# Optimization experiments

Measured on AMD Instinct MI355X. Metric: run time of the kernel, lower is better.

Reference implementation:

```python
import jax, jax.numpy as jnp
import numpy as np

B, LS, LL = 1024, 128, 2048
E, VOCAB = 16, 160000
NH, KD = 8, 6
LSH_DIM, TOPK = 16, 48
D_ITEM = 3 * E  # 48
EPS = 1e-3  # keras LayerNormalization default epsilon


def setup_inputs() -> dict:
    key = jax.random.key(0)
    ks = iter(jax.random.split(key, 64))
    def nk():
        return next(ks)
    def ids(shape):
        return jax.random.randint(nk(), shape, 0, VOCAB, dtype=jnp.int32)
    inp = {}
    for n in ['uid', 'utag1', 'utag2', 'utag3', 'utag4',
              'label_goods_ids', 'label_shop_ids', 'label_cate_ids']:
        inp[n] = ids((B,))
    for n in ['shortterm_goods_ids', 'shortterm_shop_ids', 'shortterm_cate_ids']:
        inp[n] = ids((B, LS))
    for n in ['longterm_goods_ids', 'longterm_shop_ids', 'longterm_cate_ids']:
        inp[n] = ids((B, LL))
    def rn(shape, s=0.05):
        return (jax.random.normal(nk(), shape) * s).astype(jnp.float32)
    inp['emb_table'] = rn((VOCAB, E))
    inp['H'] = rn((D_ITEM, LSH_DIM), 1.0)  # non-trainable random projection
    for p in ('s', 'l'):
        inp[p + 'Wq'] = rn((D_ITEM, NH, KD)); inp[p + 'bq'] = jnp.zeros((NH, KD), jnp.float32)
        inp[p + 'Wk'] = rn((D_ITEM, NH, KD)); inp[p + 'bk'] = jnp.zeros((NH, KD), jnp.float32)
        inp[p + 'Wv'] = rn((D_ITEM, NH, KD)); inp[p + 'bv'] = jnp.zeros((NH, KD), jnp.float32)
        inp[p + 'Wo'] = rn((NH, KD, D_ITEM)); inp[p + 'bo'] = jnp.zeros((D_ITEM,), jnp.float32)
    Din = D_ITEM + 5 * E + D_ITEM + D_ITEM  # 224
    inp['W1'] = rn((Din, 200)); inp['b1'] = jnp.zeros((200,), jnp.float32)
    inp['g1'] = jnp.ones((200,), jnp.float32); inp['be1'] = jnp.zeros((200,), jnp.float32)
    inp['W2'] = rn((200, 80)); inp['b2'] = jnp.zeros((80,), jnp.float32)
    inp['g2'] = jnp.ones((80,), jnp.float32); inp['be2'] = jnp.zeros((80,), jnp.float32)
    inp['W3'] = rn((80, 1)); inp['b3'] = jnp.zeros((1,), jnp.float32)
    return inp


def _ln(x, g, b):
    m = jnp.mean(x, axis=-1, keepdims=True)
    v = jnp.mean((x - m) ** 2, axis=-1, keepdims=True)
    return (x - m) * jax.lax.rsqrt(v + EPS) * g + b


def _mha(q, kv, mask3, Wq, bq, Wk, bk, Wv, bv, Wo, bo):
    # q: [B,1,D], kv: [B,K,D], mask3: [B,1,K] float (1=keep)
    qh = jnp.einsum('bqe,ehd->bqhd', q, Wq) + bq
    kh = jnp.einsum('bke,ehd->bkhd', kv, Wk) + bk
    vh = jnp.einsum('bke,ehd->bkhd', kv, Wv) + bv
    sc = jnp.einsum('bqhd,bkhd->bhqk', qh, kh) / jnp.sqrt(jnp.float32(KD))
    sc = sc + (1.0 - mask3[:, None, :, :]) * jnp.float32(-1e9)
    a = jax.nn.softmax(sc, axis=-1)
    o = jnp.einsum('bhqk,bkhd->bqhd', a, vh)
    return jnp.einsum('bqhd,hde->bqe', o, Wo) + bo


def reference(uid, utag1, utag2, utag3, utag4,
              label_goods_ids, label_shop_ids, label_cate_ids,
              shortterm_goods_ids, shortterm_shop_ids, shortterm_cate_ids,
              longterm_goods_ids, longterm_shop_ids, longterm_cate_ids,
              emb_table, H,
              sWq, sbq, sWk, sbk, sWv, sbv, sWo, sbo,
              lWq, lbq, lWk, lbk, lWv, lbv, lWo, lbo,
              W1, b1, g1, be1, W2, b2, g2, be2, W3, b3):
    short_mask = shortterm_goods_ids == 0  # padding_index == 0
    long_mask = longterm_goods_ids == 0

    def stack_embed(lst):
        X = jnp.stack([t if t.ndim == 2 else t[:, None] for t in lst], axis=2)  # [B,L,F]
        Xe = emb_table[X]  # [B,L,F,E]
        return Xe.reshape(Xe.shape[0], Xe.shape[1], -1)

    X_item = stack_embed([label_goods_ids, label_shop_ids, label_cate_ids])  # [B,1,48]
    X_user = stack_embed([uid, utag1, utag2, utag3, utag4])                  # [B,1,80]
    X_short = stack_embed([shortterm_goods_ids, shortterm_shop_ids, shortterm_cate_ids])  # [B,LS,48]
    X_long = stack_embed([longterm_goods_ids, longterm_shop_ids, longterm_cate_ids])      # [B,LL,48]

    # short-term interest
    slen = jnp.sum((~short_mask).astype(jnp.int32), axis=1)
    smask = (jnp.arange(LS)[None, :] < slen[:, None]).astype(jnp.float32)[:, None, :]
    short_int = _mha(X_item, X_short, smask, sWq, sbq, sWk, sbk, sWv, sbv, sWo, sbo)[:, 0]

    # long-term interest: LSH sign-hash hamming top-k retrieval
    series_codes = jnp.sign(jnp.einsum('ble,em->blm', X_long, H))  # [B,LL,16]
    item_codes = jnp.sign(jnp.einsum('ble,em->blm', X_item, H))    # [B,1,16]
    scores = jnp.sum((series_codes == item_codes).astype(jnp.float32), axis=-1)  # [B,LL]
    scores = jnp.where(long_mask, -jnp.inf, scores)
    _, idx = jax.lax.top_k(scores, TOPK)  # descending, padded entries last
    top_emb = jnp.take_along_axis(X_long, idx[:, :, None], axis=1)  # [B,TOPK,48]
    top_mask = jnp.take_along_axis(long_mask, idx, axis=1)
    llen = jnp.sum((~top_mask).astype(jnp.int32), axis=1)
    lmask = (jnp.arange(TOPK)[None, :] < llen[:, None]).astype(jnp.float32)[:, None, :]
    long_int = _mha(X_item, top_emb, lmask, lWq, lbq, lWk, lbk, lWv, lbv, lWo, lbo)[:, 0]

    x = jnp.concatenate([X_item[:, 0], X_user[:, 0], short_int, long_int], axis=1)  # [B,224]
    h1 = jax.nn.relu(_ln(x @ W1 + b1, g1, be1))
    h2 = jax.nn.relu(_ln(h1 @ W2 + b2, g2, be2))
    out = jax.nn.sigmoid(h2 @ W3 + b3)  # [B,1]
    return out
```

## Files before the change

### kernel.cpp

```cpp
#include <hip/hip_runtime.h>
#include <math.h>

#define BB 1024
#define LSx 128
#define LLx 2048
#define TOPKx 48

__global__ __launch_bounds__(256, 8) void k_score(
    const int* __restrict__ lg, const int* __restrict__ lsh, const int* __restrict__ lc,
    const int* __restrict__ ig, const int* __restrict__ ish, const int* __restrict__ ici,
    const float* __restrict__ emb, const float* __restrict__ Hm,
    signed char* __restrict__ gsc)
{
  __shared__ float Xitem[48];
  __shared__ int icode[16];
  __shared__ float4 xsh[256][4];
  const int b = blockIdx.y, tid = threadIdx.x;

  const int l = blockIdx.x * 256 + tid;
  const size_t off = (size_t)b * LLx + l;
  const int gid = lg[off];

  if (tid < 48) {
    const int seg = tid >> 4, e = tid & 15;
    const int id = (seg == 0) ? ig[b] : (seg == 1) ? ish[b] : ici[b];
    Xitem[tid] = emb[(size_t)id * 16 + e];
  }
  __syncthreads();
  if (tid < 16) {
    float dd = 0.f;
    for (int e = 0; e < 48; ++e) dd += Xitem[e] * Hm[e * 16 + tid];
    icode[tid] = (dd > 0.f) ? 1 : (dd < 0.f ? -1 : 0);
  }

  float d[16];
  #pragma unroll
  for (int m = 0; m < 16; ++m) d[m] = 0.f;

  const int srow = tid >> 2;
  const int q = tid & 3;
  const size_t bbase = (size_t)b * LLx + (size_t)blockIdx.x * 256;

  #pragma unroll
  for (int seg = 0; seg < 3; ++seg) {
    const int* idarr = (seg == 0) ? lg : (seg == 1) ? lsh : lc;
    #pragma unroll
    for (int jj = 0; jj < 4; ++jj) {
      const int pos = jj * 64 + srow;
      const int id = idarr[bbase + pos];
      const float4 v = *(const float4*)(emb + (size_t)id * 16 + q * 4);
      xsh[pos][q ^ ((pos >> 1) & 3)] = v;
    }
    __syncthreads();
    if (gid != 0) {
      float x[16];
      #pragma unroll
      for (int qq = 0; qq < 4; ++qq) {
        const float4 r = xsh[tid][qq ^ ((tid >> 1) & 3)];
        x[qq * 4 + 0] = r.x; x[qq * 4 + 1] = r.y;
        x[qq * 4 + 2] = r.z; x[qq * 4 + 3] = r.w;
      }
      const float* hb = Hm + seg * 256;
      #pragma unroll
      for (int i = 0; i < 16; ++i) {
        const float xi = x[i];
        #pragma unroll
        for (int mc = 0; mc < 4; ++mc) {
          const float4 h4 = *(const float4*)(hb + i * 16 + mc * 4);
          d[mc * 4 + 0] += xi * h4.x;
          d[mc * 4 + 1] += xi * h4.y;
          d[mc * 4 + 2] += xi * h4.z;
          d[mc * 4 + 3] += xi * h4.w;
        }
      }
    }
    if (seg < 2) __syncthreads();
  }

  int sc = -1;
  if (gid != 0) {
    sc = 0;
    #pragma unroll
    for (int m = 0; m < 16; ++m) {
      const int cs = (d[m] > 0.f) ? 1 : (d[m] < 0.f ? -1 : 0);
      sc += (cs == icode[m]) ? 1 : 0;
    }
  }
  gsc[off] = (signed char)sc;
}

template<int K, int STRIDE, bool IS_LONG>
__global__ __launch_bounds__(128) void k_mha(
    const int* __restrict__ kg, const int* __restrict__ ks, const int* __restrict__ kc,
    const int* __restrict__ ig, const int* __restrict__ ish, const int* __restrict__ ici,
    const float* __restrict__ emb,
    const float* __restrict__ Wq, const float* __restrict__ bq,
    const float* __restrict__ Wk, const float* __restrict__ bk,
    const float* __restrict__ Wv, const float* __restrict__ bv,
    const float* __restrict__ Wo, const float* __restrict__ bo,
    const int* __restrict__ sel,
    float* __restrict__ outv)
{
  __shared__ float Xitem[48];
  __shared__ float qh[48];
  __shared__ __align__(16) float vhs[K][48];
  __shared__ float scs[8][K + 4];
  __shared__ float osm[48];
  __shared__ unsigned char validf[K];
  const int b = blockIdx.x, tid = threadIdx.x;

  if (tid < 48) {
    const int seg = tid >> 4, e = tid & 15;
    const int id = (seg == 0) ? ig[b] : (seg == 1) ? ish[b] : ici[b];
    Xitem[tid] = emb[(size_t)id * 16 + e];
  }
  __syncthreads();
  if (tid < 48) {
    float a = bq[tid];
    for (int e = 0; e < 48; ++e) a += Xitem[e] * Wq[e * 48 + tid];
    qh[tid] = a;
  }

  int gid = 0, sid = 0, cid = 0;
  if (tid < K) {
    const int pos = IS_LONG ? sel[b * TOPKx + tid] : tid;
    const size_t off = (size_t)b * STRIDE + pos;
    gid = kg[off]; sid = ks[off]; cid = kc[off];
  }
  const int nval = __syncthreads_count((tid < K) && (gid != 0));

  if (tid < K) {
    validf[tid] = IS_LONG ? (unsigned char)(gid != 0) : (unsigned char)(tid < nval);
    float kh[48], vh[48];
    #pragma unroll
    for (int j = 0; j < 48; ++j) { kh[j] = bk[j]; vh[j] = bv[j]; }
    const int ids3[3] = {gid, sid, cid};
    #pragma unroll
    for (int seg = 0; seg < 3; ++seg) {
      const float* row = emb + (size_t)ids3[seg] * 16;
      #pragma unroll
      for (int i4 = 0; i4 < 4; ++i4) {
        const float4 xv = ((const float4*)row)[i4];
        const float xs[4] = {xv.x, xv.y, xv.z, xv.w};
        #pragma unroll
        for (int c = 0; c < 4; ++c) {
          const int e = seg * 16 + i4 * 4 + c;
          const float* wkr = Wk + e * 48;
          const float* wvr = Wv + e * 48;
          const float xe = xs[c];
          #pragma unroll
          for (int j = 0; j < 48; ++j) {
            kh[j] += xe * wkr[j];
            vh[j] += xe * wvr[j];
          }
        }
      }
    }
    #pragma unroll
    for (int h = 0; h < 8; ++h) {
      float s = 0.f;
      #pragma unroll
      for (int d = 0; d < 6; ++d) s += qh[h * 6 + d] * kh[h * 6 + d];
      scs[h][tid] = s * 0.40824829046386301637f;
    }
    #pragma unroll
    for (int j = 0; j < 48; ++j) vhs[tid][j] = vh[j];
  }
  __syncthreads();

  {
    const int h = tid >> 4, l16 = tid & 15;
    float amax = -INFINITY;
    for (int k = l16; k < K; k += 16) if (validf[k]) amax = fmaxf(amax, scs[h][k]);
    #pragma unroll
    for (int m = 1; m < 16; m <<= 1) amax = fmaxf(amax, __shfl_xor(amax, m, 16));
    if (nval == 0) {
      for (int k = l16; k < K; k += 16) scs[h][k] = 1.0f / (float)K;
    } else {
      float ssum = 0.f;
      for (int k = l16; k < K; k += 16) {
        const float ev = validf[k] ? expf(scs[h][k] - amax) : 0.f;
        scs[h][k] = ev;
        ssum += ev;
      }
      #pragma unroll
      for (int m = 1; m < 16; m <<= 1) ssum += __shfl_xor(ssum, m, 16);
      const float inv = 1.0f / ssum;
      for (int k = l16; k < K; k += 16) scs[h][k] *= inv;
    }
  }
  __syncthreads();

  if (tid < 48) {
    const int h = tid / 6;
    float a = 0.f;
    for (int k = 0; k < K; ++k) a += scs[h][k] * vhs[k][tid];
    osm[tid] = a;
  }
  __syncthreads();
  if (tid < 48) {
    float r = bo[tid];
    for (int j = 0; j < 48; ++j) r += osm[j] * Wo[j * 48 + tid];
    outv[b * 48 + tid] = r;
  }
}

__global__ __launch_bounds__(256) void k_mha_long(
    const int* __restrict__ kg, const int* __restrict__ ks, const int* __restrict__ kc,
    const int* __restrict__ ig, const int* __restrict__ ish, const int* __restrict__ ici,
    const float* __restrict__ emb,
    const float* __restrict__ Wq, const float* __restrict__ bq,
    const float* __restrict__ Wk, const float* __restrict__ bk,
    const float* __restrict__ Wv, const float* __restrict__ bv,
    const float* __restrict__ Wo, const float* __restrict__ bo,
    const signed char* __restrict__ gsc,
    float* __restrict__ outv)
{
  __shared__ int hist[18];
  __shared__ int cnt_above;
  __shared__ int wsum[4];
  __shared__ int selsh[TOPKx];
  __shared__ float Xitem[48];
  __shared__ float qh[48];
  __shared__ __align__(16) float vhs[TOPKx][48];
  __shared__ float scs[8][TOPKx + 4];
  __shared__ float osm[48];
  __shared__ unsigned char validf[TOPKx];
  const int b = blockIdx.x, tid = threadIdx.x;

  const int2 myv = ((const int2*)(gsc + (size_t)b * LLx))[tid];
  signed char loc[8];
  *(int2*)loc = myv;

  if (tid < 18) hist[tid] = 0;
  if (tid == 0) cnt_above = 0;
  if (tid < 48) {
    const int seg = tid >> 4, e = tid & 15;
    const int id = (seg == 0) ? ig[b] : (seg == 1) ? ish[b] : ici[b];
    Xitem[tid] = emb[(size_t)id * 16 + e];
  }
  __syncthreads();

  #pragma unroll
  for (int j = 0; j < 8; ++j) atomicAdd(&hist[(int)loc[j] + 1], 1);
  if (tid < 48) {
    float a = bq[tid];
    for (int e = 0; e < 48; ++e) a += Xitem[e] * Wq[e * 48 + tid];
    qh[tid] = a;
  }
  __syncthreads();

  int above = 0, tval = -1, need = 0;
  for (int s = 16; s >= -1; --s) {
    const int c = hist[s + 1];
    if (above + c >= TOPKx) { tval = s; need = TOPKx - above; break; }
    above += c;
  }

  const int base_l = tid * (LLx / 256);
  int cnt = 0;
  #pragma unroll
  for (int j = 0; j < 8; ++j) cnt += ((int)loc[j] == tval) ? 1 : 0;
  int v = cnt;
  const int lane = tid & 63, wave = tid >> 6;
  #pragma unroll
  for (int o = 1; o < 64; o <<= 1) {
    const int u = __shfl_up(v, o, 64);
    if (lane >= o) v += u;
  }
  if (lane == 63) wsum[wave] = v;
  __syncthreads();
  int rank = v - cnt;
  for (int w = 0; w < wave; ++w) rank += wsum[w];

  #pragma unroll
  for (int j = 0; j < 8; ++j) {
    const int l = base_l + j;
    const int s = (int)loc[j];
    if (s > tval) {
      const int slot = atomicAdd(&cnt_above, 1);
      selsh[slot] = l;
    } else if (s == tval) {
      if (rank < need) selsh[above + rank] = l;
      ++rank;
    }
  }
  __syncthreads();

  int gid = 0, sid = 0, cid = 0;
  if (tid < TOPKx) {
    const int pos = selsh[tid];
    const size_t off = (size_t)b * LLx + pos;
    gid = kg[off]; sid = ks[off]; cid = kc[off];
  }
  const int nval = __syncthreads_count((tid < TOPKx) && (gid != 0));

  if (tid < TOPKx) {
    validf[tid] = (unsigned char)(gid != 0);
    float kh[48], vh[48];
    #pragma unroll
    for (int j = 0; j < 48; ++j) { kh[j] = bk[j]; vh[j] = bv[j]; }
    const int ids3[3] = {gid, sid, cid};
    #pragma unroll
    for (int seg = 0; seg < 3; ++seg) {
      const float* row = emb + (size_t)ids3[seg] * 16;
      #pragma unroll
      for (int i4 = 0; i4 < 4; ++i4) {
        const float4 xv = ((const float4*)row)[i4];
        const float xs[4] = {xv.x, xv.y, xv.z, xv.w};
        #pragma unroll
        for (int c = 0; c < 4; ++c) {
          const int e = seg * 16 + i4 * 4 + c;
          const float* wkr = Wk + e * 48;
          const float* wvr = Wv + e * 48;
          const float xe = xs[c];
          #pragma unroll
          for (int j = 0; j < 48; ++j) {
            kh[j] += xe * wkr[j];
            vh[j] += xe * wvr[j];
          }
        }
      }
    }
    #pragma unroll
    for (int h = 0; h < 8; ++h) {
      float s = 0.f;
      #pragma unroll
      for (int d = 0; d < 6; ++d) s += qh[h * 6 + d] * kh[h * 6 + d];
      scs[h][tid] = s * 0.40824829046386301637f;
    }
    #pragma unroll
    for (int j = 0; j < 48; ++j) vhs[tid][j] = vh[j];
  }
  __syncthreads();

  if (tid < 128) {
    const int h = tid >> 4, l16 = tid & 15;
    float amax = -INFINITY;
    for (int k = l16; k < TOPKx; k += 16) if (validf[k]) amax = fmaxf(amax, scs[h][k]);
    #pragma unroll
    for (int m = 1; m < 16; m <<= 1) amax = fmaxf(amax, __shfl_xor(amax, m, 16));
    if (nval == 0) {
      for (int k = l16; k < TOPKx; k += 16) scs[h][k] = 1.0f / (float)TOPKx;
    } else {
      float ssum = 0.f;
      for (int k = l16; k < TOPKx; k += 16) {
        const float ev = validf[k] ? expf(scs[h][k] - amax) : 0.f;
        scs[h][k] = ev;
        ssum += ev;
      }
      #pragma unroll
      for (int m = 1; m < 16; m <<= 1) ssum += __shfl_xor(ssum, m, 16);
      const float inv = 1.0f / ssum;
      for (int k = l16; k < TOPKx; k += 16) scs[h][k] *= inv;
    }
  }
  __syncthreads();

  if (tid < 48) {
    const int h = tid / 6;
    float a = 0.f;
    for (int k = 0; k < TOPKx; ++k) a += scs[h][k] * vhs[k][tid];
    osm[tid] = a;
  }
  __syncthreads();
  if (tid < 48) {
    float r = bo[tid];
    for (int j = 0; j < 48; ++j) r += osm[j] * Wo[j * 48 + tid];
    outv[b * 48 + tid] = r;
  }
}

__device__ __forceinline__ float block_sum256(float v, float* red) {
  #pragma unroll
  for (int m = 32; m >= 1; m >>= 1) v += __shfl_xor(v, m, 64);
  const int lane = threadIdx.x & 63, wave = threadIdx.x >> 6;
  if (lane == 0) red[wave] = v;
  __syncthreads();
  const float t = red[0] + red[1] + red[2] + red[3];
  __syncthreads();
  return t;
}

__global__ __launch_bounds__(256) void k_mlp(
    const int* __restrict__ uid, const int* __restrict__ u1, const int* __restrict__ u2,
    const int* __restrict__ u3, const int* __restrict__ u4,
    const int* __restrict__ ig, const int* __restrict__ ish, const int* __restrict__ ici,
    const float* __restrict__ emb,
    const float* __restrict__ sint, const float* __restrict__ lint,
    const float* __restrict__ W1, const float* __restrict__ b1,
    const float* __restrict__ g1, const float* __restrict__ be1,
    const float* __restrict__ W2, const float* __restrict__ b2,
    const float* __restrict__ g2, const float* __restrict__ be2,
    const float* __restrict__ W3, const float* __restrict__ b3,
    float* __restrict__ out)
{
  __shared__ __align__(16) float x[224];
  __shared__ __align__(16) float h1[200];
  __shared__ float h2[80];
  __shared__ float red[4];
  const int b = blockIdx.x, tid = threadIdx.x;

  if (tid < 128) {
    const int e = tid & 15;
    int id;
    if (tid < 48) {
      const int seg = tid >> 4;
      id = (seg == 0) ? ig[b] : (seg == 1) ? ish[b] : ici[b];
    } else {
      const int f = (tid - 48) >> 4;
      id = (f == 0) ? uid[b] : (f == 1) ? u1[b] : (f == 2) ? u2[b] : (f == 3) ? u3[b] : u4[b];
    }
    x[tid] = emb[(size_t)id * 16 + e];
  } else if (tid < 176) {
    x[tid] = sint[b * 48 + (tid - 128)];
  } else if (tid < 224) {
    x[tid] = lint[b * 48 + (tid - 176)];
  }
  __syncthreads();

  float v = 0.f;
  if (tid < 200) {
    v = b1[tid];
    for (int i4 = 0; i4 < 56; ++i4) {
      const float4 xv = *(const float4*)(x + i4 * 4);
      const float* w = W1 + i4 * 4 * 200 + tid;
      v += xv.x * w[0];
      v += xv.y * w[200];
      v += xv.z * w[400];
      v += xv.w * w[600];
    }
  }
  const float mean1 = block_sum256((tid < 200) ? v : 0.f, red) * (1.0f / 200.0f);
  const float dv = (tid < 200) ? (v - mean1) : 0.f;
  const float var1 = block_sum256(dv * dv, red) * (1.0f / 200.0f);
  if (tid < 200) {
    const float y = (v - mean1) * rsqrtf(var1 + 1e-3f) * g1[tid] + be1[tid];
    h1[tid] = fmaxf(y, 0.f);
  }
  __syncthreads();

  float v2 = 0.f;
  if (tid < 80) {
    v2 = b2[tid];
    for (int i4 = 0; i4 < 50; ++i4) {
      const float4 xv = *(const float4*)(h1 + i4 * 4);
      const float* w = W2 + i4 * 4 * 80 + tid;
      v2 += xv.x * w[0];
      v2 += xv.y * w[80];
      v2 += xv.z * w[160];
      v2 += xv.w * w[240];
    }
  }
  const float mean2 = block_sum256((tid < 80) ? v2 : 0.f, red) * (1.0f / 80.0f);
  const float dv2 = (tid < 80) ? (v2 - mean2) : 0.f;
  const float var2 = block_sum256(dv2 * dv2, red) * (1.0f / 80.0f);
  if (tid < 80) {
    const float y = (v2 - mean2) * rsqrtf(var2 + 1e-3f) * g2[tid] + be2[tid];
    h2[tid] = fmaxf(y, 0.f);
  }
  __syncthreads();

  const float p = (tid < 80) ? h2[tid] * W3[tid] : 0.f;
  const float z = block_sum256(p, red);
  if (tid == 0) {
    out[b] = 1.0f / (1.0f + expf(-(z + b3[0])));
  }
}

extern "C" void kernel_launch(void* const* d_in, const int* in_sizes, int n_in,
                              void* d_out, int out_size, void* d_ws, size_t ws_size,
                              hipStream_t stream) {
  (void)in_sizes; (void)n_in; (void)out_size; (void)ws_size;
  const int* uid = (const int*)d_in[0];
  const int* u1  = (const int*)d_in[1];
  const int* u2  = (const int*)d_in[2];
  const int* u3  = (const int*)d_in[3];
  const int* u4  = (const int*)d_in[4];
  const int* ig  = (const int*)d_in[5];
  const int* ish = (const int*)d_in[6];
  const int* ici = (const int*)d_in[7];
  const int* sg  = (const int*)d_in[8];
  const int* ss  = (const int*)d_in[9];
  const int* scd = (const int*)d_in[10];
  const int* lg  = (const int*)d_in[11];
  const int* ls  = (const int*)d_in[12];
  const int* lcd = (const int*)d_in[13];
  const float* emb = (const float*)d_in[14];
  const float* Hm  = (const float*)d_in[15];
  const float* sWq = (const float*)d_in[16];
  const float* sbq = (const float*)d_in[17];
  const float* sWk = (const float*)d_in[18];
  const float* sbk = (const float*)d_in[19];
  const float* sWv = (const float*)d_in[20];
  const float* sbv = (const float*)d_in[21];
  const float* sWo = (const float*)d_in[22];
  const float* sbo = (const float*)d_in[23];
  const float* lWq = (const float*)d_in[24];
  const float* lbq = (const float*)d_in[25];
  const float* lWk = (const float*)d_in[26];
  const float* lbk = (const float*)d_in[27];
  const float* lWv = (const float*)d_in[28];
  const float* lbv = (const float*)d_in[29];
  const float* lWo = (const float*)d_in[30];
  const float* lbo = (const float*)d_in[31];
  const float* W1 = (const float*)d_in[32];
  const float* b1 = (const float*)d_in[33];
  const float* g1 = (const float*)d_in[34];
  const float* be1 = (const float*)d_in[35];
  const float* W2 = (const float*)d_in[36];
  const float* b2 = (const float*)d_in[37];
  const float* g2 = (const float*)d_in[38];
  const float* be2 = (const float*)d_in[39];
  const float* W3 = (const float*)d_in[40];
  const float* b3 = (const float*)d_in[41];
  float* out = (float*)d_out;

  signed char* gsc = (signed char*)d_ws;
  float* sint = (float*)((char*)d_ws + (size_t)BB * LLx);
  float* lint = sint + BB * 48;

  k_score<<<dim3(LLx / 256, BB), dim3(256), 0, stream>>>(
      lg, ls, lcd, ig, ish, ici, emb, Hm, gsc);
  k_mha<128, 128, false><<<dim3(BB), dim3(128), 0, stream>>>(
      sg, ss, scd, ig, ish, ici, emb,
      sWq, sbq, sWk, sbk, sWv, sbv, sWo, sbo, (const int*)nullptr, sint);
  k_mha_long<<<dim3(BB), dim3(256), 0, stream>>>(
      lg, ls, lcd, ig, ish, ici, emb,
      lWq, lbq, lWk, lbk, lWv, lbv, lWo, lbo, gsc, lint);
  k_mlp<<<dim3(BB), dim3(256), 0, stream>>>(
      uid, u1, u2, u3, u4, ig, ish, ici, emb,
      sint, lint, W1, b1, g1, be1, W2, b2, g2, be2, W3, b3, out);
}
```

Measured before the change: 354.2 us.

## Prefetch next segment gathers in scoring and split K/V projection across more threads

In the LSH scoring kernel, the embedding gathers for the next segment are now issued into registers before the current segment's projection is computed. This overlaps gather latency with the matmul, and the occupancy hint in the launch bounds is dropped to make room for the extra registers. The short-term MHA kernel goes from 128 to 256 threads, with each half computing 24 of the 48 K/V columns. The long-term MHA kernel uses all 4 wave-groups of 64 threads to compute 12 columns each instead of letting only 48 threads work. This cuts per-thread serial work and register pressure, at the cost of redundant embedding-row loads across thread groups.

```diff
diff --git a/kernel.cpp b/kernel.cpp
--- a/kernel.cpp
+++ b/kernel.cpp
@@ -6,7 +6,7 @@
 #define LLx 2048
 #define TOPKx 48
 
-__global__ __launch_bounds__(256, 8) void k_score(
+__global__ __launch_bounds__(256) void k_score(
     const int* __restrict__ lg, const int* __restrict__ lsh, const int* __restrict__ lc,
     const int* __restrict__ ig, const int* __restrict__ ish, const int* __restrict__ ici,
     const float* __restrict__ emb, const float* __restrict__ Hm,
@@ -33,25 +33,39 @@
     icode[tid] = (dd > 0.f) ? 1 : (dd < 0.f ? -1 : 0);
   }
 
-  float d[16];
-  #pragma unroll
-  for (int m = 0; m < 16; ++m) d[m] = 0.f;
-
   const int srow = tid >> 2;
   const int q = tid & 3;
   const size_t bbase = (size_t)b * LLx + (size_t)blockIdx.x * 256;
 
+  float4 stage[4];
+  #pragma unroll
+  for (int jj = 0; jj < 4; ++jj) {
+    const int pos = jj * 64 + srow;
+    const int id = lg[bbase + pos];
+    stage[jj] = *(const float4*)(emb + (size_t)id * 16 + q * 4);
+  }
+
+  float d[16];
+  #pragma unroll
+  for (int m = 0; m < 16; ++m) d[m] = 0.f;
+
   #pragma unroll
   for (int seg = 0; seg < 3; ++seg) {
-    const int* idarr = (seg == 0) ? lg : (seg == 1) ? lsh : lc;
     #pragma unroll
     for (int jj = 0; jj < 4; ++jj) {
       const int pos = jj * 64 + srow;
-      const int id = idarr[bbase + pos];
-      const float4 v = *(const float4*)(emb + (size_t)id * 16 + q * 4);
-      xsh[pos][q ^ ((pos >> 1) & 3)] = v;
+      xsh[pos][q ^ ((pos >> 1) & 3)] = stage[jj];
     }
     __syncthreads();
+    if (seg < 2) {
+      const int* idn = (seg == 0) ? lsh : lc;
+      #pragma unroll
+      for (int jj = 0; jj < 4; ++jj) {
+        const int pos = jj * 64 + srow;
+        const int id = idn[bbase + pos];
+        stage[jj] = *(const float4*)(emb + (size_t)id * 16 + q * 4);
+      }
+    }
     if (gid != 0) {
       float x[16];
       #pragma unroll
@@ -89,8 +103,7 @@
   gsc[off] = (signed char)sc;
 }
 
-template<int K, int STRIDE, bool IS_LONG>
-__global__ __launch_bounds__(128) void k_mha(
+__global__ __launch_bounds__(256) void k_mha_short(
     const int* __restrict__ kg, const int* __restrict__ ks, const int* __restrict__ kc,
     const int* __restrict__ ig, const int* __restrict__ ish, const int* __restrict__ ici,
     const float* __restrict__ emb,
@@ -98,16 +111,17 @@
     const float* __restrict__ Wk, const float* __restrict__ bk,
     const float* __restrict__ Wv, const float* __restrict__ bv,
     const float* __restrict__ Wo, const float* __restrict__ bo,
-    const int* __restrict__ sel,
     float* __restrict__ outv)
 {
   __shared__ float Xitem[48];
   __shared__ float qh[48];
-  __shared__ __align__(16) float vhs[K][48];
-  __shared__ float scs[8][K + 4];
+  __shared__ __align__(16) float vhs[LSx][48];
+  __shared__ float scs[8][LSx + 4];
   __shared__ float osm[48];
-  __shared__ unsigned char validf[K];
+  __shared__ unsigned char validf[LSx];
   const int b = blockIdx.x, tid = threadIdx.x;
+  const int w = tid >> 7;
+  const int k = tid & 127;
 
   if (tid < 48) {
     const int seg = tid >> 4, e = tid & 15;
@@ -121,19 +135,19 @@
     qh[tid] = a;
   }
 
-  int gid = 0, sid = 0, cid = 0;
-  if (tid < K) {
-    const int pos = IS_LONG ? sel[b * TOPKx + tid] : tid;
-    const size_t off = (size_t)b * STRIDE + pos;
+  int gid, sid, cid;
+  {
+    const size_t off = (size_t)b * LSx + k;
     gid = kg[off]; sid = ks[off]; cid = kc[off];
   }
-  const int nval = __syncthreads_count((tid < K) && (gid != 0));
-
-  if (tid < K) {
-    validf[tid] = IS_LONG ? (unsigned char)(gid != 0) : (unsigned char)(tid < nval);
-    float kh[48], vh[48];
-    #pragma unroll
-    for (int j = 0; j < 48; ++j) { kh[j] = bk[j]; vh[j] = bv[j]; }
+  const int nval = __syncthreads_count((w == 0) && (gid != 0));
+  if (w == 0) validf[k] = (unsigned char)(k < nval);
+
+  {
+    const int cb = w * 24;
+    float kh[24], vh[24];
+    #pragma unroll
+    for (int j = 0; j < 24; ++j) { kh[j] = bk[cb + j]; vh[j] = bv[cb + j]; }
     const int ids3[3] = {gid, sid, cid};
     #pragma unroll
     for (int seg = 0; seg < 3; ++seg) {
@@ -145,11 +159,11 @@
         #pragma unroll
         for (int c = 0; c < 4; ++c) {
           const int e = seg * 16 + i4 * 4 + c;
-          const float* wkr = Wk + e * 48;
-          const float* wvr = Wv + e * 48;
+          const float* wkr = Wk + e * 48 + cb;
+          const float* wvr = Wv + e * 48 + cb;
           const float xe = xs[c];
           #pragma unroll
-          for (int j = 0; j < 48; ++j) {
+          for (int j = 0; j < 24; ++j) {
             kh[j] += xe * wkr[j];
             vh[j] += xe * wvr[j];
           }
@@ -157,36 +171,37 @@
       }
     }
     #pragma unroll
-    for (int h = 0; h < 8; ++h) {
+    for (int hh = 0; hh < 4; ++hh) {
+      const int h = w * 4 + hh;
       float s = 0.f;
       #pragma unroll
-      for (int d = 0; d < 6; ++d) s += qh[h * 6 + d] * kh[h * 6 + d];
-      scs[h][tid] = s * 0.40824829046386301637f;
-    }
-    #pragma unroll
-    for (int j = 0; j < 48; ++j) vhs[tid][j] = vh[j];
-  }
-  __syncthreads();
-
-  {
+      for (int d = 0; d < 6; ++d) s += qh[h * 6 + d] * kh[hh * 6 + d];
+      scs[h][k] = s * 0.40824829046386301637f;
+    }
+    #pragma unroll
+    for (int j = 0; j < 24; ++j) vhs[k][cb + j] = vh[j];
+  }
+  __syncthreads();
+
+  if (tid < 128) {
     const int h = tid >> 4, l16 = tid & 15;
     float amax = -INFINITY;
-    for (int k = l16; k < K; k += 16) if (validf[k]) amax = fmaxf(amax, scs[h][k]);
+    for (int kk = l16; kk < LSx; kk += 16) if (validf[kk]) amax = fmaxf(amax, scs[h][kk]);
     #pragma unroll
     for (int m = 1; m < 16; m <<= 1) amax = fmaxf(amax, __shfl_xor(amax, m, 16));
     if (nval == 0) {
-      for (int k = l16; k < K; k += 16) scs[h][k] = 1.0f / (float)K;
+      for (int kk = l16; kk < LSx; kk += 16) scs[h][kk] = 1.0f / (float)LSx;
     } else {
       float ssum = 0.f;
-      for (int k = l16; k < K; k += 16) {
-        const float ev = validf[k] ? expf(scs[h][k] - amax) : 0.f;
-        scs[h][k] = ev;
+      for (int kk = l16; kk < LSx; kk += 16) {
+        const float ev = validf[kk] ? expf(scs[h][kk] - amax) : 0.f;
+        scs[h][kk] = ev;
         ssum += ev;
       }
       #pragma unroll
       for (int m = 1; m < 16; m <<= 1) ssum += __shfl_xor(ssum, m, 16);
       const float inv = 1.0f / ssum;
-      for (int k = l16; k < K; k += 16) scs[h][k] *= inv;
+      for (int kk = l16; kk < LSx; kk += 16) scs[h][kk] *= inv;
     }
   }
   __syncthreads();
@@ -194,7 +209,7 @@
   if (tid < 48) {
     const int h = tid / 6;
     float a = 0.f;
-    for (int k = 0; k < K; ++k) a += scs[h][k] * vhs[k][tid];
+    for (int k2 = 0; k2 < LSx; ++k2) a += scs[h][k2] * vhs[k2][tid];
     osm[tid] = a;
   }
   __syncthreads();
@@ -287,19 +302,22 @@
   }
   __syncthreads();
 
+  const int g = tid >> 6;
+  const int kk = tid & 63;
   int gid = 0, sid = 0, cid = 0;
-  if (tid < TOPKx) {
-    const int pos = selsh[tid];
+  if (kk < TOPKx) {
+    const int pos = selsh[kk];
     const size_t off = (size_t)b * LLx + pos;
     gid = kg[off]; sid = ks[off]; cid = kc[off];
   }
-  const int nval = __syncthreads_count((tid < TOPKx) && (gid != 0));
-
-  if (tid < TOPKx) {
-    validf[tid] = (unsigned char)(gid != 0);
-    float kh[48], vh[48];
-    #pragma unroll
-    for (int j = 0; j < 48; ++j) { kh[j] = bk[j]; vh[j] = bv[j]; }
+  const int nval = __syncthreads_count((g == 0) && (kk < TOPKx) && (gid != 0));
+
+  if (kk < TOPKx) {
+    if (g == 0) validf[kk] = (unsigned char)(gid != 0);
+    const int cb = g * 12;
+    float kh[12], vh[12];
+    #pragma unroll
+    for (int j = 0; j < 12; ++j) { kh[j] = bk[cb + j]; vh[j] = bv[cb + j]; }
     const int ids3[3] = {gid, sid, cid};
     #pragma unroll
     for (int seg = 0; seg < 3; ++seg) {
@@ -311,11 +329,11 @@
         #pragma unroll
         for (int c = 0; c < 4; ++c) {
           const int e = seg * 16 + i4 * 4 + c;
-          const float* wkr = Wk + e * 48;
-          const float* wvr = Wv + e * 48;
+          const float* wkr = Wk + e * 48 + cb;
+          const float* wvr = Wv + e * 48 + cb;
           const float xe = xs[c];
           #pragma unroll
-          for (int j = 0; j < 48; ++j) {
+          for (int j = 0; j < 12; ++j) {
             kh[j] += xe * wkr[j];
             vh[j] += xe * wvr[j];
           }
@@ -323,14 +341,15 @@
       }
     }
     #pragma unroll
-    for (int h = 0; h < 8; ++h) {
+    for (int hh = 0; hh < 2; ++hh) {
+      const int h = g * 2 + hh;
       float s = 0.f;
       #pragma unroll
-      for (int d = 0; d < 6; ++d) s += qh[h * 6 + d] * kh[h * 6 + d];
-      scs[h][tid] = s * 0.40824829046386301637f;
-    }
-    #pragma unroll
-    for (int j = 0; j < 48; ++j) vhs[tid][j] = vh[j];
+      for (int d = 0; d < 6; ++d) s += qh[h * 6 + d] * kh[hh * 6 + d];
+      scs[h][kk] = s * 0.40824829046386301637f;
+    }
+    #pragma unroll
+    for (int j = 0; j < 12; ++j) vhs[kk][cb + j] = vh[j];
   }
   __syncthreads();
 
@@ -522,9 +541,9 @@
 
   k_score<<<dim3(LLx / 256, BB), dim3(256), 0, stream>>>(
       lg, ls, lcd, ig, ish, ici, emb, Hm, gsc);
-  k_mha<128, 128, false><<<dim3(BB), dim3(128), 0, stream>>>(
+  k_mha_short<<<dim3(BB), dim3(256), 0, stream>>>(
       sg, ss, scd, ig, ish, ici, emb,
-      sWq, sbq, sWk, sbk, sWv, sbv, sWo, sbo, (const int*)nullptr, sint);
+      sWq, sbq, sWk, sbk, sWv, sbv, sWo, sbo, sint);
   k_mha_long<<<dim3(BB), dim3(256), 0, stream>>>(
       lg, ls, lcd, ig, ish, ici, emb,
       lWq, lbq, lWk, lbk, lWv, lbv, lWo, lbo, gsc, lint);
```

Result: slower. 482.9 us (+36.3%).

## Split MHA kernels per head, separate top-k kernel, fold output projection into MLP

Applied to the files above, without the earlier changes.

The attention kernels are re-gridded to one block per (batch, head), so each thread keeps only 6 key/value accumulators instead of 48. This cuts register pressure and raises parallelism. Top-k selection moves into its own kernel that writes indices to global memory, and the Wo output projection moves into the MLP kernel. k_score drops the XOR swizzle in favour of a padded shared array and relaxes its launch bounds occupancy hint. The trade-off is one extra launch, recomputing the per-head query in every block, and extra global traffic for the selection indices.

```diff
diff --git a/kernel.cpp b/kernel.cpp
--- a/kernel.cpp
+++ b/kernel.cpp
@@ -6,7 +6,7 @@
 #define LLx 2048
 #define TOPKx 48
 
-__global__ __launch_bounds__(256, 8) void k_score(
+__global__ __launch_bounds__(256, 2) void k_score(
     const int* __restrict__ lg, const int* __restrict__ lsh, const int* __restrict__ lc,
     const int* __restrict__ ig, const int* __restrict__ ish, const int* __restrict__ ici,
     const float* __restrict__ emb, const float* __restrict__ Hm,
@@ -14,7 +14,7 @@
 {
   __shared__ float Xitem[48];
   __shared__ int icode[16];
-  __shared__ float4 xsh[256][4];
+  __shared__ __align__(16) float4 xsh[256][5];
   const int b = blockIdx.y, tid = threadIdx.x;
 
   const int l = blockIdx.x * 256 + tid;
@@ -33,14 +33,14 @@
     icode[tid] = (dd > 0.f) ? 1 : (dd < 0.f ? -1 : 0);
   }
 
-  float d[16];
-  #pragma unroll
-  for (int m = 0; m < 16; ++m) d[m] = 0.f;
-
   const int srow = tid >> 2;
   const int q = tid & 3;
   const size_t bbase = (size_t)b * LLx + (size_t)blockIdx.x * 256;
 
+  float d[16];
+  #pragma unroll
+  for (int m = 0; m < 16; ++m) d[m] = 0.f;
+
   #pragma unroll
   for (int seg = 0; seg < 3; ++seg) {
     const int* idarr = (seg == 0) ? lg : (seg == 1) ? lsh : lc;
@@ -48,15 +48,14 @@
     for (int jj = 0; jj < 4; ++jj) {
       const int pos = jj * 64 + srow;
       const int id = idarr[bbase + pos];
-      const float4 v = *(const float4*)(emb + (size_t)id * 16 + q * 4);
-      xsh[pos][q ^ ((pos >> 1) & 3)] = v;
+      xsh[pos][q] = *(const float4*)(emb + (size_t)id * 16 + q * 4);
     }
     __syncthreads();
     if (gid != 0) {
       float x[16];
       #pragma unroll
       for (int qq = 0; qq < 4; ++qq) {
-        const float4 r = xsh[tid][qq ^ ((tid >> 1) & 3)];
+        const float4 r = xsh[tid][qq];
         x[qq * 4 + 0] = r.x; x[qq * 4 + 1] = r.y;
         x[qq * 4 + 2] = r.z; x[qq * 4 + 3] = r.w;
       }
@@ -89,25 +88,78 @@
   gsc[off] = (signed char)sc;
 }
 
-template<int K, int STRIDE, bool IS_LONG>
-__global__ __launch_bounds__(128) void k_mha(
+__global__ __launch_bounds__(256) void k_topk(
+    const signed char* __restrict__ gsc, int* __restrict__ sel)
+{
+  __shared__ int hist[18];
+  __shared__ int cnt_above;
+  __shared__ int wsum[4];
+  const int b = blockIdx.x, tid = threadIdx.x;
+
+  const int2 myv = ((const int2*)(gsc + (size_t)b * LLx))[tid];
+  signed char loc[8];
+  *(int2*)loc = myv;
+
+  if (tid < 18) hist[tid] = 0;
+  if (tid == 0) cnt_above = 0;
+  __syncthreads();
+
+  #pragma unroll
+  for (int j = 0; j < 8; ++j) atomicAdd(&hist[(int)loc[j] + 1], 1);
+  __syncthreads();
+
+  int above = 0, tval = -1, need = 0;
+  for (int s = 16; s >= -1; --s) {
+    const int c = hist[s + 1];
+    if (above + c >= TOPKx) { tval = s; need = TOPKx - above; break; }
+    above += c;
+  }
+
+  const int base_l = tid * (LLx / 256);
+  int cnt = 0;
+  #pragma unroll
+  for (int j = 0; j < 8; ++j) cnt += ((int)loc[j] == tval) ? 1 : 0;
+  int v = cnt;
+  const int lane = tid & 63, wave = tid >> 6;
+  #pragma unroll
+  for (int o = 1; o < 64; o <<= 1) {
+    const int u = __shfl_up(v, o, 64);
+    if (lane >= o) v += u;
+  }
+  if (lane == 63) wsum[wave] = v;
+  __syncthreads();
+  int rank = v - cnt;
+  for (int w = 0; w < wave; ++w) rank += wsum[w];
+
+  #pragma unroll
+  for (int j = 0; j < 8; ++j) {
+    const int l = base_l + j;
+    const int s = (int)loc[j];
+    if (s > tval) {
+      const int slot = atomicAdd(&cnt_above, 1);
+      sel[b * TOPKx + slot] = l;
+    } else if (s == tval) {
+      if (rank < need) sel[b * TOPKx + above + rank] = l;
+      ++rank;
+    }
+  }
+}
+
+__global__ __launch_bounds__(128) void k_mha_short_h(
     const int* __restrict__ kg, const int* __restrict__ ks, const int* __restrict__ kc,
     const int* __restrict__ ig, const int* __restrict__ ish, const int* __restrict__ ici,
     const float* __restrict__ emb,
     const float* __restrict__ Wq, const float* __restrict__ bq,
     const float* __restrict__ Wk, const float* __restrict__ bk,
     const float* __restrict__ Wv, const float* __restrict__ bv,
-    const float* __restrict__ Wo, const float* __restrict__ bo,
-    const int* __restrict__ sel,
-    float* __restrict__ outv)
+    float* __restrict__ osm_g)
 {
   __shared__ float Xitem[48];
-  __shared__ float qh[48];
-  __shared__ __align__(16) float vhs[K][48];
-  __shared__ float scs[8][K + 4];
-  __shared__ float osm[48];
-  __shared__ unsigned char validf[K];
-  const int b = blockIdx.x, tid = threadIdx.x;
+  __shared__ float qh[6];
+  __shared__ float scs[LSx];
+  __shared__ float vhT[6][LSx + 4];
+  __shared__ unsigned char validf[LSx];
+  const int b = blockIdx.x, h = blockIdx.y, tid = threadIdx.x;
 
   if (tid < 48) {
     const int seg = tid >> 4, e = tid & 15;
@@ -115,25 +167,25 @@
     Xitem[tid] = emb[(size_t)id * 16 + e];
   }
   __syncthreads();
-  if (tid < 48) {
-    float a = bq[tid];
-    for (int e = 0; e < 48; ++e) a += Xitem[e] * Wq[e * 48 + tid];
+  if (tid < 6) {
+    const int col = h * 6 + tid;
+    float a = bq[col];
+    for (int e = 0; e < 48; ++e) a += Xitem[e] * Wq[e * 48 + col];
     qh[tid] = a;
   }
 
-  int gid = 0, sid = 0, cid = 0;
-  if (tid < K) {
-    const int pos = IS_LONG ? sel[b * TOPKx + tid] : tid;
-    const size_t off = (size_t)b * STRIDE + pos;
+  int gid, sid, cid;
+  {
+    const size_t off = (size_t)b * LSx + tid;
     gid = kg[off]; sid = ks[off]; cid = kc[off];
   }
-  const int nval = __syncthreads_count((tid < K) && (gid != 0));
-
-  if (tid < K) {
-    validf[tid] = IS_LONG ? (unsigned char)(gid != 0) : (unsigned char)(tid < nval);
-    float kh[48], vh[48];
-    #pragma unroll
-    for (int j = 0; j < 48; ++j) { kh[j] = bk[j]; vh[j] = bv[j]; }
+  const int nval = __syncthreads_count(gid != 0);
+
+  {
+    validf[tid] = (unsigned char)(tid < nval);
+    float kh[6], vh[6];
+    #pragma unroll
+    for (int j = 0; j < 6; ++j) { kh[j] = bk[h * 6 + j]; vh[j] = bv[h * 6 + j]; }
     const int ids3[3] = {gid, sid, cid};
     #pragma unroll
     for (int seg = 0; seg < 3; ++seg) {
@@ -145,151 +197,89 @@
         #pragma unroll
         for (int c = 0; c < 4; ++c) {
           const int e = seg * 16 + i4 * 4 + c;
-          const float* wkr = Wk + e * 48;
-          const float* wvr = Wv + e * 48;
+          const float* wkr = Wk + e * 48 + h * 6;
+          const float* wvr = Wv + e * 48 + h * 6;
           const float xe = xs[c];
           #pragma unroll
-          for (int j = 0; j < 48; ++j) {
+          for (int j = 0; j < 6; ++j) {
             kh[j] += xe * wkr[j];
             vh[j] += xe * wvr[j];
           }
         }
       }
     }
-    #pragma unroll
-    for (int h = 0; h < 8; ++h) {
-      float s = 0.f;
-      #pragma unroll
-      for (int d = 0; d < 6; ++d) s += qh[h * 6 + d] * kh[h * 6 + d];
-      scs[h][tid] = s * 0.40824829046386301637f;
-    }
-    #pragma unroll
-    for (int j = 0; j < 48; ++j) vhs[tid][j] = vh[j];
-  }
-  __syncthreads();
-
-  {
-    const int h = tid >> 4, l16 = tid & 15;
+    float s = 0.f;
+    #pragma unroll
+    for (int d = 0; d < 6; ++d) s += qh[d] * kh[d];
+    scs[tid] = s * 0.40824829046386301637f;
+    #pragma unroll
+    for (int j = 0; j < 6; ++j) vhT[j][tid] = vh[j];
+  }
+  __syncthreads();
+
+  if (tid < 16) {
+    const int l16 = tid;
     float amax = -INFINITY;
-    for (int k = l16; k < K; k += 16) if (validf[k]) amax = fmaxf(amax, scs[h][k]);
+    for (int k = l16; k < LSx; k += 16) if (validf[k]) amax = fmaxf(amax, scs[k]);
     #pragma unroll
     for (int m = 1; m < 16; m <<= 1) amax = fmaxf(amax, __shfl_xor(amax, m, 16));
     if (nval == 0) {
-      for (int k = l16; k < K; k += 16) scs[h][k] = 1.0f / (float)K;
+      for (int k = l16; k < LSx; k += 16) scs[k] = 1.0f / (float)LSx;
     } else {
       float ssum = 0.f;
-      for (int k = l16; k < K; k += 16) {
-        const float ev = validf[k] ? expf(scs[h][k] - amax) : 0.f;
-        scs[h][k] = ev;
+      for (int k = l16; k < LSx; k += 16) {
+        const float ev = validf[k] ? expf(scs[k] - amax) : 0.f;
+        scs[k] = ev;
         ssum += ev;
       }
       #pragma unroll
       for (int m = 1; m < 16; m <<= 1) ssum += __shfl_xor(ssum, m, 16);
       const float inv = 1.0f / ssum;
-      for (int k = l16; k < K; k += 16) scs[h][k] *= inv;
-    }
-  }
-  __syncthreads();
-
-  if (tid < 48) {
-    const int h = tid / 6;
+      for (int k = l16; k < LSx; k += 16) scs[k] *= inv;
+    }
+  }
+  __syncthreads();
+
+  if (tid < 6) {
     float a = 0.f;
-    for (int k = 0; k < K; ++k) a += scs[h][k] * vhs[k][tid];
-    osm[tid] = a;
-  }
-  __syncthreads();
-  if (tid < 48) {
-    float r = bo[tid];
-    for (int j = 0; j < 48; ++j) r += osm[j] * Wo[j * 48 + tid];
-    outv[b * 48 + tid] = r;
-  }
-}
-
-__global__ __launch_bounds__(256) void k_mha_long(
+    for (int k = 0; k < LSx; ++k) a += scs[k] * vhT[tid][k];
+    osm_g[b * 48 + h * 6 + tid] = a;
+  }
+}
+
+__global__ __launch_bounds__(64) void k_mha_long_h(
     const int* __restrict__ kg, const int* __restrict__ ks, const int* __restrict__ kc,
     const int* __restrict__ ig, const int* __restrict__ ish, const int* __restrict__ ici,
     const float* __restrict__ emb,
     const float* __restrict__ Wq, const float* __restrict__ bq,
     const float* __restrict__ Wk, const float* __restrict__ bk,
     const float* __restrict__ Wv, const float* __restrict__ bv,
-    const float* __restrict__ Wo, const float* __restrict__ bo,
-    const signed char* __restrict__ gsc,
-    float* __restrict__ outv)
+    const int* __restrict__ sel,
+    float* __restrict__ osm_g)
 {
-  __shared__ int hist[18];
-  __shared__ int cnt_above;
-  __shared__ int wsum[4];
-  __shared__ int selsh[TOPKx];
   __shared__ float Xitem[48];
-  __shared__ float qh[48];
-  __shared__ __align__(16) float vhs[TOPKx][48];
-  __shared__ float scs[8][TOPKx + 4];
-  __shared__ float osm[48];
+  __shared__ float qh[6];
+  __shared__ float scs[TOPKx];
+  __shared__ float vhT[6][TOPKx + 4];
   __shared__ unsigned char validf[TOPKx];
-  const int b = blockIdx.x, tid = threadIdx.x;
-
-  const int2 myv = ((const int2*)(gsc + (size_t)b * LLx))[tid];
-  signed char loc[8];
-  *(int2*)loc = myv;
-
-  if (tid < 18) hist[tid] = 0;
-  if (tid == 0) cnt_above = 0;
+  const int b = blockIdx.x, h = blockIdx.y, tid = threadIdx.x;
+
   if (tid < 48) {
     const int seg = tid >> 4, e = tid & 15;
     const int id = (seg == 0) ? ig[b] : (seg == 1) ? ish[b] : ici[b];
     Xitem[tid] = emb[(size_t)id * 16 + e];
   }
   __syncthreads();
-
-  #pragma unroll
-  for (int j = 0; j < 8; ++j) atomicAdd(&hist[(int)loc[j] + 1], 1);
-  if (tid < 48) {
-    float a = bq[tid];
-    for (int e = 0; e < 48; ++e) a += Xitem[e] * Wq[e * 48 + tid];
+  if (tid < 6) {
+    const int col = h * 6 + tid;
+    float a = bq[col];
+    for (int e = 0; e < 48; ++e) a += Xitem[e] * Wq[e * 48 + col];
     qh[tid] = a;
   }
-  __syncthreads();
-
-  int above = 0, tval = -1, need = 0;
-  for (int s = 16; s >= -1; --s) {
-    const int c = hist[s + 1];
-    if (above + c >= TOPKx) { tval = s; need = TOPKx - above; break; }
-    above += c;
-  }
-
-  const int base_l = tid * (LLx / 256);
-  int cnt = 0;
-  #pragma unroll
-  for (int j = 0; j < 8; ++j) cnt += ((int)loc[j] == tval) ? 1 : 0;
-  int v = cnt;
-  const int lane = tid & 63, wave = tid >> 6;
-  #pragma unroll
-  for (int o = 1; o < 64; o <<= 1) {
-    const int u = __shfl_up(v, o, 64);
-    if (lane >= o) v += u;
-  }
-  if (lane == 63) wsum[wave] = v;
-  __syncthreads();
-  int rank = v - cnt;
-  for (int w = 0; w < wave; ++w) rank += wsum[w];
-
-  #pragma unroll
-  for (int j = 0; j < 8; ++j) {
-    const int l = base_l + j;
-    const int s = (int)loc[j];
-    if (s > tval) {
-      const int slot = atomicAdd(&cnt_above, 1);
-      selsh[slot] = l;
-    } else if (s == tval) {
-      if (rank < need) selsh[above + rank] = l;
-      ++rank;
-    }
-  }
-  __syncthreads();
 
   int gid = 0, sid = 0, cid = 0;
   if (tid < TOPKx) {
-    const int pos = selsh[tid];
+    const int pos = sel[b * TOPKx + tid];
     const size_t off = (size_t)b * LLx + pos;
     gid = kg[off]; sid = ks[off]; cid = kc[off];
   }
@@ -297,9 +287,9 @@
 
   if (tid < TOPKx) {
     validf[tid] = (unsigned char)(gid != 0);
-    float kh[48], vh[48];
-    #pragma unroll
-    for (int j = 0; j < 48; ++j) { kh[j] = bk[j]; vh[j] = bv[j]; }
+    float kh[6], vh[6];
+    #pragma unroll
+    for (int j = 0; j < 6; ++j) { kh[j] = bk[h * 6 + j]; vh[j] = bv[h * 6 + j]; }
     const int ids3[3] = {gid, sid, cid};
     #pragma unroll
     for (int seg = 0; seg < 3; ++seg) {
@@ -311,63 +301,53 @@
         #pragma unroll
         for (int c = 0; c < 4; ++c) {
           const int e = seg * 16 + i4 * 4 + c;
-          const float* wkr = Wk + e * 48;
-          const float* wvr = Wv + e * 48;
+          const float* wkr = Wk + e * 48 + h * 6;
+          const float* wvr = Wv + e * 48 + h * 6;
           const float xe = xs[c];
           #pragma unroll
-          for (int j = 0; j < 48; ++j) {
+          for (int j = 0; j < 6; ++j) {
             kh[j] += xe * wkr[j];
             vh[j] += xe * wvr[j];
           }
         }
       }
     }
-    #pragma unroll
-    for (int h = 0; h < 8; ++h) {
-      float s = 0.f;
-      #pragma unroll
-      for (int d = 0; d < 6; ++d) s += qh[h * 6 + d] * kh[h * 6 + d];
-      scs[h][tid] = s * 0.40824829046386301637f;
-    }
-    #pragma unroll
-    for (int j = 0; j < 48; ++j) vhs[tid][j] = vh[j];
-  }
-  __syncthreads();
-
-  if (tid < 128) {
-    const int h = tid >> 4, l16 = tid & 15;
+    float s = 0.f;
+    #pragma unroll
+    for (int d = 0; d < 6; ++d) s += qh[d] * kh[d];
+    scs[tid] = s * 0.40824829046386301637f;
+    #pragma unroll
+    for (int j = 0; j < 6; ++j) vhT[j][tid] = vh[j];
+  }
+  __syncthreads();
+
+  if (tid < 16) {
+    const int l16 = tid;
     float amax = -INFINITY;
-    for (int k = l16; k < TOPKx; k += 16) if (validf[k]) amax = fmaxf(amax, scs[h][k]);
+    for (int k = l16; k < TOPKx; k += 16) if (validf[k]) amax = fmaxf(amax, scs[k]);
     #pragma unroll
     for (int m = 1; m < 16; m <<= 1) amax = fmaxf(amax, __shfl_xor(amax, m, 16));
     if (nval == 0) {
-      for (int k = l16; k < TOPKx; k += 16) scs[h][k] = 1.0f / (float)TOPKx;
+      for (int k = l16; k < TOPKx; k += 16) scs[k] = 1.0f / (float)TOPKx;
     } else {
       float ssum = 0.f;
       for (int k = l16; k < TOPKx; k += 16) {
-        const float ev = validf[k] ? expf(scs[h][k] - amax) : 0.f;
-        scs[h][k] = ev;
+        const float ev = validf[k] ? expf(scs[k] - amax) : 0.f;
+        scs[k] = ev;
         ssum += ev;
       }
       #pragma unroll
       for (int m = 1; m < 16; m <<= 1) ssum += __shfl_xor(ssum, m, 16);
       const float inv = 1.0f / ssum;
-      for (int k = l16; k < TOPKx; k += 16) scs[h][k] *= inv;
-    }
-  }
-  __syncthreads();
-
-  if (tid < 48) {
-    const int h = tid / 6;
+      for (int k = l16; k < TOPKx; k += 16) scs[k] *= inv;
+    }
+  }
+  __syncthreads();
+
+  if (tid < 6) {
     float a = 0.f;
-    for (int k = 0; k < TOPKx; ++k) a += scs[h][k] * vhs[k][tid];
-    osm[tid] = a;
-  }
-  __syncthreads();
-  if (tid < 48) {
-    float r = bo[tid];
-    for (int j = 0; j < 48; ++j) r += osm[j] * Wo[j * 48 + tid];
-    outv[b * 48 + tid] = r;
+    for (int k = 0; k < TOPKx; ++k) a += scs[k] * vhT[tid][k];
+    osm_g[b * 48 + h * 6 + tid] = a;
   }
 }
 
@@ -387,7 +367,9 @@
     const int* __restrict__ u3, const int* __restrict__ u4,
     const int* __restrict__ ig, const int* __restrict__ ish, const int* __restrict__ ici,
     const float* __restrict__ emb,
-    const float* __restrict__ sint, const float* __restrict__ lint,
+    const float* __restrict__ osm_s, const float* __restrict__ osm_l,
+    const float* __restrict__ sWo, const float* __restrict__ sbo,
+    const float* __restrict__ lWo, const float* __restrict__ lbo,
     const float* __restrict__ W1, const float* __restrict__ b1,
     const float* __restrict__ g1, const float* __restrict__ be1,
     const float* __restrict__ W2, const float* __restrict__ b2,
@@ -399,6 +381,7 @@
   __shared__ __align__(16) float h1[200];
   __shared__ float h2[80];
   __shared__ float red[4];
+  __shared__ float osm_sl[48], osm_ll[48];
   const int b = blockIdx.x, tid = threadIdx.x;
 
   if (tid < 128) {
@@ -413,9 +396,21 @@
     }
     x[tid] = emb[(size_t)id * 16 + e];
   } else if (tid < 176) {
-    x[tid] = sint[b * 48 + (tid - 128)];
+    osm_sl[tid - 128] = osm_s[b * 48 + (tid - 128)];
   } else if (tid < 224) {
-    x[tid] = lint[b * 48 + (tid - 176)];
+    osm_ll[tid - 176] = osm_l[b * 48 + (tid - 176)];
+  }
+  __syncthreads();
+
+  if (tid < 48) {
+    float r = sbo[tid];
+    for (int j = 0; j < 48; ++j) r += osm_sl[j] * sWo[j * 48 + tid];
+    x[128 + tid] = r;
+  } else if (tid >= 64 && tid < 112) {
+    const int c = tid - 64;
+    float r = lbo[c];
+    for (int j = 0; j < 48; ++j) r += osm_ll[j] * lWo[j * 48 + c];
+    x[176 + c] = r;
   }
   __syncthreads();
 
@@ -517,18 +512,21 @@
   float* out = (float*)d_out;
 
   signed char* gsc = (signed char*)d_ws;
-  float* sint = (float*)((char*)d_ws + (size_t)BB * LLx);
-  float* lint = sint + BB * 48;
+  int* sel = (int*)((char*)d_ws + (size_t)BB * LLx);
+  float* osm_s = (float*)(sel + BB * TOPKx);
+  float* osm_l = osm_s + BB * 48;
 
   k_score<<<dim3(LLx / 256, BB), dim3(256), 0, stream>>>(
       lg, ls, lcd, ig, ish, ici, emb, Hm, gsc);
-  k_mha<128, 128, false><<<dim3(BB), dim3(128), 0, stream>>>(
+  k_topk<<<dim3(BB), dim3(256), 0, stream>>>(gsc, sel);
+  k_mha_short_h<<<dim3(BB, 8), dim3(128), 0, stream>>>(
       sg, ss, scd, ig, ish, ici, emb,
-      sWq, sbq, sWk, sbk, sWv, sbv, sWo, sbo, (const int*)nullptr, sint);
-  k_mha_long<<<dim3(BB), dim3(256), 0, stream>>>(
+      sWq, sbq, sWk, sbk, sWv, sbv, osm_s);
+  k_mha_long_h<<<dim3(BB, 8), dim3(64), 0, stream>>>(
       lg, ls, lcd, ig, ish, ici, emb,
-      lWq, lbq, lWk, lbk, lWv, lbv, lWo, lbo, gsc, lint);
+      lWq, lbq, lWk, lbk, lWv, lbv, sel, osm_l);
   k_mlp<<<dim3(BB), dim3(256), 0, stream>>>(
       uid, u1, u2, u3, u4, ig, ish, ici, emb,
-      sint, lint, W1, b1, g1, be1, W2, b2, g2, be2, W3, b3, out);
-}
+      osm_s, osm_l, sWo, sbo, lWo, lbo,
+      W1, b1, g1, be1, W2, b2, g2, be2, W3, b3, out);
+}
```

Result: faster. 317.7 us (-10.3%).
